# Kernel tuning notes

Hardware: AMD Instinct MI355X
Metric: run time of the kernel (lower is better)

## Reference

```python
import jax, jax.numpy as jnp
import numpy as np
from math import comb

# --- module hyperparameters (from init_kwargs / module-level constants) ---
F = 32          # features
NITER = 3       # num_iterations
NB = 16         # num_basis_functions
NDCM = 4        # n_dcm
CUTOFF = 4.0
MAXZ = 17       # max_atomic_number
NC = 9          # (max_degree+1)^2 spherical components, max_degree=2
DEG = np.array([0, 1, 1, 1, 2, 2, 2, 2, 2])  # degree l of each component
BINOM = jnp.asarray([comb(NB - 1, k) for k in range(NB)], dtype=jnp.float32)


def _np_sph9(x, y, z):
    # real spherical harmonics up to l=2 on the unit sphere (numpy, for Gaunt table)
    c0 = 0.28209479177387814; c1 = 0.4886025119029199
    c2a = 1.0925484305920792; c2b = 0.31539156525252005; c2c = 0.5462742152960396
    return np.stack([c0 * np.ones_like(x), c1 * y, c1 * z, c1 * x,
                     c2a * x * y, c2a * y * z, c2b * (3.0 * z * z - 1.0),
                     c2a * x * z, c2c * (x * x - y * y)], axis=0)


def _gaunt():
    # real Gaunt (Clebsch-Gordan-type) coefficients G[a,b,c] = int Y_a Y_b Y_c dOmega
    # via Gauss-Legendre (cos theta) x midpoint (phi) quadrature -- exact for l<=2 products
    ct, wt = np.polynomial.legendre.leggauss(64)
    nph = 256
    phi = (np.arange(nph) + 0.5) * (2.0 * np.pi / nph)
    st = np.sqrt(1.0 - ct ** 2)
    x = st[:, None] * np.cos(phi)[None, :]
    y = st[:, None] * np.sin(phi)[None, :]
    z = np.broadcast_to(ct[:, None], x.shape)
    w = (wt[:, None] * (2.0 * np.pi / nph)) * np.ones((1, nph))
    Y = _np_sph9(x, y, z)
    G = np.einsum('aij,bij,cij,ij->abc', Y, Y, Y, w)
    G[np.abs(G) < 1e-6] = 0.0
    return G

CG = jnp.asarray(_gaunt(), dtype=jnp.float32)  # (9, 9, 9), sparse


def _sph9(u):
    # u: (E, 3) unit vectors -> (E, 9)
    x, y, z = u[:, 0], u[:, 1], u[:, 2]
    c0 = 0.28209479177387814; c1 = 0.4886025119029199
    c2a = 1.0925484305920792; c2b = 0.31539156525252005; c2c = 0.5462742152960396
    return jnp.stack([jnp.full_like(x, c0), c1 * y, c1 * z, c1 * x,
                      c2a * x * y, c2a * y * z, c2b * (3.0 * z * z - 1.0),
                      c2a * x * z, c2c * (x * x - y * y)], axis=-1)


def _radial(r):
    # reciprocal Bernstein radial basis * smooth cutoff; r: (E,) -> (E, NB)
    u = 1.0 / (1.0 + r)
    k = jnp.arange(NB, dtype=jnp.float32)
    rb = BINOM * u[:, None] ** k * (1.0 - u[:, None]) ** (NB - 1 - k)
    t = r / CUTOFF
    den = jnp.where(t < 1.0, 1.0 - t * t, 1.0)
    fc = jnp.where(t < 1.0, jnp.exp(-t * t / den), 0.0)  # smooth_cutoff
    return rb * fc[:, None]


def _equiv_dense(x, W, b=None):
    # per-degree linear (equivariant Dense): x (N, 9, Fin), W (3, Fin, Fout); bias on l=0 only
    y = jnp.einsum('ncf,cfg->ncg', x, W[DEG])
    if b is not None:
        y = y.at[:, 0, :].add(b)
    return y


def _tp(xs, bf):
    # Gaunt tensor-product contraction: out[e,c,f] = sum_ab CG[a,b,c] xs[e,a,f] bf[e,b,f]
    # loop over the 9 fixed output components to avoid an (E,9,9,F) intermediate
    out = []
    for c in range(NC):
        t = jnp.einsum('eaf,ab->ebf', xs, CG[:, :, c])
        out.append(jnp.sum(t * bf, axis=1))
    return jnp.stack(out, axis=1)


def _forward(atomic_numbers, positions, dst_idx, src_idx, embed, Wb, W1, b1, W2, b2,
             Wt00, Wt11, Wmono, element_bias):
    n = atomic_numbers.shape[0]
    disp = positions[src_idx] - positions[dst_idx]                 # (E, 3) gather
    r = jnp.sqrt(jnp.sum(disp * disp, axis=-1) + 1e-12)            # safe norm
    u = disp / r[:, None]
    basis = _sph9(u)[:, :, None] * _radial(r)[:, None, :]          # (E, 9, NB)
    x = jnp.zeros((n, NC, F), dtype=positions.dtype).at[:, 0, :].set(embed[atomic_numbers])
    for i in range(NITER):  # message passing iterations
        bf = jnp.einsum('ebn,bng->ebg', basis, Wb[i][DEG])         # per-degree radial->feature mix (E,9,F)
        msg = _tp(x[src_idx], bf)                                  # gather src + tensor product
        y = x + jax.ops.segment_sum(msg, dst_idx, num_segments=n)  # scatter-aggregate + residual add
        y = _equiv_dense(y, W1[i], b1[i])
        y = jax.nn.silu(y)
        y = _equiv_dense(y, W2[i], b2[i])
        x = x + y                                                  # residual update
    # TensorDense to n_dcm channels, then readout heads
    mono = (x[:, 0, :] @ Wt00) @ Wmono + element_bias[atomic_numbers][:, None]  # (N, NDCM)
    dip = jnp.einsum('ncf,fg->ncg', x[:, 1:4, :], Wt11)            # (N, 3, NDCM) vector channel
    dip = jnp.clip(jax.nn.silu(dip), -0.3, 0.3) + positions[:, :, None]
    return mono, dip


def setup_inputs():
    key = jax.random.key(0)
    ks = jax.random.split(key, 12)
    N, E = 10000, 160000
    return {
        'atomic_numbers': jax.random.randint(ks[0], (N,), 0, MAXZ + 1),
        'positions': jax.random.normal(ks[1], (N, 3), jnp.float32) * 3.0,
        'dst_idx': jax.random.randint(ks[2], (E,), 0, N),
        'src_idx': jax.random.randint(ks[3], (E,), 0, N),
        'embed': jax.random.normal(ks[4], (MAXZ + 1, F), jnp.float32),
        'Wb': jax.random.normal(ks[5], (NITER, 3, NB, F), jnp.float32) / np.sqrt(NB).astype(np.float32),
        'W1': jax.random.normal(ks[6], (NITER, 3, F, F), jnp.float32) / np.sqrt(F).astype(np.float32),
        'b1': jnp.zeros((NITER, F), jnp.float32),
        'W2': jax.random.normal(ks[7], (NITER, 3, F, F), jnp.float32) / np.sqrt(F).astype(np.float32),
        'b2': jnp.zeros((NITER, F), jnp.float32),
        'Wt00': jax.random.normal(ks[8], (F, NDCM), jnp.float32) / np.sqrt(F).astype(np.float32),
        'Wt11': jax.random.normal(ks[9], (F, NDCM), jnp.float32) / np.sqrt(F).astype(np.float32),
        'Wmono': jax.random.normal(ks[10], (NDCM, NDCM), jnp.float32) / np.sqrt(NDCM).astype(np.float32),
        'element_bias': jnp.zeros((MAXZ + 1,), jnp.float32),
    }


def reference(atomic_numbers, positions, dst_idx, src_idx, embed, Wb, W1, b1, W2, b2,
              Wt00, Wt11, Wmono, element_bias):
    return _forward(atomic_numbers, positions, dst_idx, src_idx, embed, Wb, W1, b1, W2, b2,
                    Wt00, Wt11, Wmono, element_bias)
```

## Files before the change

kernel.cpp:

```cpp
#include <hip/hip_runtime.h>
#include <hip/hip_bf16.h>


#define NITER 3
#define BCAP  64

#define OFF_WB    0
#define OFF_W1    4608
#define OFF_B1    13824
#define OFF_W2    13920
#define OFF_B2    23136
#define OFF_WT00  23232
#define OFF_WT11  23360
#define OFF_WMONO 23488
#define OFF_EB    23504
#define OFF_EMB   23522
#define WC_TOTAL  24098

__device__ __forceinline__ float b2f(const __hip_bfloat16 v) { return __bfloat162float(v); }

#define KC0 0.28209479177387814f
#define KG1 0.21850968611841584f
#define KG2 0.12615662610100802f
#define KG3 0.18022375157287861f
#define KG4 0.09011187578643931f
#define KG5 0.15607834722743988f

__device__ __forceinline__ float ldany(const void* p, int i, bool f32) {
    return f32 ? ((const float*)p)[i] : b2f(((const __hip_bfloat16*)p)[i]);
}

__device__ __forceinline__ bool wave_sniff(const void* pos) {
    const __hip_bfloat16* p = (const __hip_bfloat16*)pos;
    int lane = threadIdx.x & 63;
    int bad = 0;
    #pragma unroll
    for (int k = 0; k < 4; k++) {
        float v = b2f(p[lane + k*64]);
        bad |= !(fabsf(v) < 1.0e6f);
    }
    return __ballot(bad) != 0ull;
}

__device__ __forceinline__ float xadd32(float v) {
    return v + __int_as_float(__shfl_xor(__float_as_int(v), 32, 64));
}

__device__ __forceinline__ bool edge_geom(float dx, float dy, float dz,
                                          float* sp, float* rad) {
    float r2 = dx*dx + dy*dy + dz*dz + 1e-12f;
    if (r2 >= 16.0f) return false;
    float r  = sqrtf(r2);
    float t2 = r2 * 0.0625f;
    float fc = __expf(-t2 / (1.0f - t2));
    float u = 1.0f / (1.0f + r);
    float v = 1.0f - u;
    const float BIN[16] = {1.f,15.f,105.f,455.f,1365.f,3003.f,5005.f,6435.f,
                           6435.f,5005.f,3003.f,1365.f,455.f,105.f,15.f,1.f};
    float vp[16];
    vp[0] = 1.0f;
    #pragma unroll
    for (int k = 1; k < 16; k++) vp[k] = vp[k-1] * v;
    float up = 1.0f;
    #pragma unroll
    for (int n = 0; n < 16; n++) { rad[n] = BIN[n] * up * vp[15-n] * fc; up *= u; }
    float ir = 1.0f / r;
    float ux = dx*ir, uy = dy*ir, uz = dz*ir;
    const float c0 = 0.28209479177387814f, c1 = 0.4886025119029199f;
    const float c2a = 1.0925484305920792f, c2b = 0.31539156525252005f, c2c = 0.5462742152960396f;
    sp[0] = c0;
    sp[1] = c1*uy; sp[2] = c1*uz; sp[3] = c1*ux;
    sp[4] = c2a*ux*uy; sp[5] = c2a*uy*uz; sp[6] = c2b*(3.0f*uz*uz - 1.0f);
    sp[7] = c2a*ux*uz; sp[8] = c2c*(ux*ux - uy*uy);
    return true;
}

__device__ __forceinline__ void write_geo_slot(float* gp, int s,
                                               const float* sp, const float* rad) {
    float4* g4 = (float4*)gp;
    g4[0] = make_float4(__int_as_float(s), 0.f, sp[0], sp[1]);
    g4[1] = make_float4(sp[2], sp[3], sp[4], sp[5]);
    g4[2] = make_float4(sp[6], sp[7], sp[8], 0.f);
    g4[4] = make_float4(rad[0],  rad[1],  rad[2],  rad[3]);
    g4[5] = make_float4(rad[4],  rad[5],  rad[6],  rad[7]);
    g4[6] = make_float4(rad[8],  rad[9],  rad[10], rad[11]);
    g4[7] = make_float4(rad[12], rad[13], rad[14], rad[15]);
}

template <bool FIRST, bool LAST>
__global__ __launch_bounds__(256) void iter_kernel(
        const float* __restrict__ xin, float* __restrict__ xout,
        const float* __restrict__ geo2, const int* __restrict__ cur,
        const float* __restrict__ Wbi,
        const float* __restrict__ W1i, const float* __restrict__ b1i,
        const float* __restrict__ W2i, const float* __restrict__ b2i,
        const int* __restrict__ an, const float* __restrict__ posf,
        const float* __restrict__ wc, const void* __restrict__ pos,
        void* __restrict__ out_, int N) {
    constexpr int NCH = LAST ? 4 : 9;
    constexpr int NR  = LAST ? 2 : 5;
    __shared__ float sm[4][9][33];
    bool f32o = false;
    if (LAST) f32o = wave_sniff(pos);
    int tid   = threadIdx.x;
    int wslot = tid >> 6;
    int lane  = tid & 63;
    int f     = lane & 31;
    int half  = lane >> 5;
    int n     = blockIdx.x * 4 + wslot;
    bool act  = (n < N);
    float (*tile)[33] = sm[wslot];

    float w0[16], w1[16], w2[16];
    #pragma unroll
    for (int k = 0; k < 16; k++) {
        w0[k] = Wbi[(0*16 + k)*32 + f];
        w1[k] = Wbi[(1*16 + k)*32 + f];
        w2[k] = Wbi[(2*16 + k)*32 + f];
    }
    float A0=0.f,A1=0.f,A2=0.f,A3=0.f,A4=0.f,A5=0.f,A6=0.f,A7=0.f,A8=0.f;
    if (act) {
        int beg = n * BCAP, end = beg + cur[n];
        for (int e = beg + half; e < end; e += 2) {
            const float4* gp = (const float4*)(geo2 + (size_t)e * 32);
            float4 h0 = gp[0], h1 = gp[1], h2 = gp[2];
            float4 r0 = gp[4], r1 = gp[5], r2 = gp[6], r3 = gp[7];
            int s = __float_as_int(h0.x);
            float rad[16] = {r0.x,r0.y,r0.z,r0.w, r1.x,r1.y,r1.z,r1.w,
                             r2.x,r2.y,r2.z,r2.w, r3.x,r3.y,r3.z,r3.w};
            float rw0 = 0.f, rw1 = 0.f, rw2 = 0.f;
            #pragma unroll
            for (int k = 0; k < 16; k++) {
                rw0 = fmaf(rad[k], w0[k], rw0);
                rw1 = fmaf(rad[k], w1[k], rw1);
                rw2 = fmaf(rad[k], w2[k], rw2);
            }
            float B0 = h0.z*rw0;
            float B1 = h0.w*rw1, B2 = h1.x*rw1, B3 = h1.y*rw1;
            float B4 = h1.z*rw2, B5 = h1.w*rw2, B6 = h2.x*rw2,
                  B7 = h2.y*rw2, B8 = h2.z*rw2;
            const float* xp = xin + (size_t)s*288 + f;
            if (FIRST) {
                float X0 = xp[0];
                float k0 = KC0 * X0;
                A0 += k0*B0; A1 += k0*B1; A2 += k0*B2; A3 += k0*B3; A4 += k0*B4;
                A5 += k0*B5; A6 += k0*B6; A7 += k0*B7; A8 += k0*B8;
            } else {
                float X0 = xp[0],   X1 = xp[32],  X2 = xp[64],  X3 = xp[96],  X4 = xp[128];
                float X5 = xp[160], X6 = xp[192], X7 = xp[224], X8 = xp[256];
                A0 += KC0*(X0*B0 + X1*B1 + X2*B2 + X3*B3 + X4*B4 + X5*B5 + X6*B6 + X7*B7 + X8*B8);
                A1 += KC0*(X0*B1 + X1*B0) + KG1*(X3*B4 + X4*B3 + X2*B5 + X5*B2)
                    - KG2*(X1*B6 + X6*B1) - KG1*(X1*B8 + X8*B1);
                A2 += KC0*(X0*B2 + X2*B0) + KG1*(X1*B5 + X5*B1 + X3*B7 + X7*B3)
                    + 2.0f*KG2*(X2*B6 + X6*B2);
                A3 += KC0*(X0*B3 + X3*B0) + KG1*(X1*B4 + X4*B1 + X2*B7 + X7*B2)
                    - KG2*(X3*B6 + X6*B3) + KG1*(X3*B8 + X8*B3);
                if (!LAST) {
                    A4 += KC0*(X0*B4 + X4*B0) + KG1*(X1*B3 + X3*B1) + KG5*(X5*B7 + X7*B5)
                        - KG3*(X4*B6 + X6*B4);
                    A5 += KC0*(X0*B5 + X5*B0) + KG1*(X1*B2 + X2*B1) + KG5*(X4*B7 + X7*B4)
                        + KG4*(X5*B6 + X6*B5) - KG5*(X5*B8 + X8*B5);
                    A6 += KC0*(X0*B6 + X6*B0) - KG2*X1*B1 + 2.0f*KG2*X2*B2 - KG2*X3*B3
                        - KG3*X4*B4 + KG4*X5*B5 + KG3*X6*B6 + KG4*X7*B7 - KG3*X8*B8;
                    A7 += KC0*(X0*B7 + X7*B0) + KG1*(X2*B3 + X3*B2) + KG5*(X4*B5 + X5*B4)
                        + KG4*(X6*B7 + X7*B6) + KG5*(X7*B8 + X8*B7);
                    A8 += KC0*(X0*B8 + X8*B0) - KG1*X1*B1 + KG1*X3*B3 - KG5*X5*B5 + KG5*X7*B7
                        - KG3*(X6*B8 + X8*B6);
                }
            }
        }
    }
    A0 = xadd32(A0); A1 = xadd32(A1); A2 = xadd32(A2); A3 = xadd32(A3);
    if (!LAST) {
        A4 = xadd32(A4); A5 = xadd32(A5); A6 = xadd32(A6);
        A7 = xadd32(A7); A8 = xadd32(A8);
    }

    float xr[9];
    #pragma unroll
    for (int c = 0; c < 9; c++) xr[c] = 0.f;
    if (act) {
        if (FIRST) {
            xr[0] = xin[(size_t)n*288 + f];
        } else {
            #pragma unroll
            for (int c = 0; c < NCH; c++) xr[c] = xin[(size_t)n*288 + c*32 + f];
        }
    }

    if (act && half == 0) {
        tile[0][f] = xr[0] + A0;
        tile[1][f] = xr[1] + A1;
        tile[2][f] = xr[2] + A2;
        tile[3][f] = xr[3] + A3;
        if (!LAST) {
            tile[4][f] = xr[4] + A4;
            tile[5][f] = xr[5] + A5;
            tile[6][f] = xr[6] + A6;
            tile[7][f] = xr[7] + A7;
            tile[8][f] = xr[8] + A8;
        }
    }
    __syncthreads();

    int g = f;
    float o1[NR];
    #pragma unroll
    for (int cc = 0; cc < NR; cc++) {
        int c  = cc*2 + half;
        int cs = (c < NCH) ? c : 0;
        int d  = (cs == 0) ? 0 : ((cs < 4) ? 1 : 2);
        const float* W1p = W1i + d * 1024;
        float acc = (c == 0) ? b1i[g] : 0.f;
        #pragma unroll
        for (int fi = 0; fi < 32; fi++)
            acc = fmaf(tile[cs][fi], W1p[fi*32 + g], acc);
        acc = acc * __builtin_amdgcn_rcpf(1.0f + __expf(-acc));
        o1[cc] = acc;
    }
    __syncthreads();
    #pragma unroll
    for (int cc = 0; cc < NR; cc++) {
        int c = cc*2 + half;
        if (c < NCH) tile[c][g] = o1[cc];
    }
    __syncthreads();

    #pragma unroll
    for (int cc = 0; cc < NR; cc++) {
        int c  = cc*2 + half;
        int cs = (c < NCH) ? c : 0;
        int d  = (cs == 0) ? 0 : ((cs < 4) ? 1 : 2);
        const float* W2p = W2i + d * 1024;
        float acc = (c == 0) ? b2i[g] : 0.f;
        #pragma unroll
        for (int fi = 0; fi < 32; fi++)
            acc = fmaf(tile[cs][fi], W2p[fi*32 + g], acc);
        float xf = xr[cs] + acc;
        if (!LAST) {
            if (act && c < NCH)
                xout[(size_t)n*288 + c*32 + g] = xf;
        } else if (act) {
            const float* WT = (c == 0) ? (wc + OFF_WT00) : (wc + OFF_WT11);
            float p0 = xf * WT[g*4 + 0];
            float p1 = xf * WT[g*4 + 1];
            float p2 = xf * WT[g*4 + 2];
            float p3 = xf * WT[g*4 + 3];
            #pragma unroll
            for (int m = 1; m <= 16; m <<= 1) {
                p0 += __shfl_xor(p0, m, 64);
                p1 += __shfl_xor(p1, m, 64);
                p2 += __shfl_xor(p2, m, 64);
                p3 += __shfl_xor(p3, m, 64);
            }
            if (g == 0) {
                if (c == 0) {
                    const float* Wmono = wc + OFF_WMONO;
                    float ebv = wc[OFF_EB + an[n]];
                    #pragma unroll
                    for (int m = 0; m < 4; m++) {
                        float a2 = ebv + p0*Wmono[0*4+m] + p1*Wmono[1*4+m]
                                       + p2*Wmono[2*4+m] + p3*Wmono[3*4+m];
                        if (f32o) ((float*)out_)[n*4 + m] = a2;
                        else ((__hip_bfloat16*)out_)[n*4 + m] = __float2bfloat16(a2);
                    }
                } else {
                    float pc = posf[n*3 + (c - 1)];
                    float pv[4] = {p0, p1, p2, p3};
                    #pragma unroll
                    for (int m = 0; m < 4; m++) {
                        float v = pv[m];
                        v = v * __builtin_amdgcn_rcpf(1.0f + __expf(-v));
                        v = fminf(fmaxf(v, -0.3f), 0.3f);
                        v += pc;
                        size_t o = (size_t)N*4 + (size_t)n*12 + (size_t)(c-1)*4 + m;
                        if (f32o) ((float*)out_)[o] = v;
                        else ((__hip_bfloat16*)out_)[o] = __float2bfloat16(v);
                    }
                }
            }
        }
    }
}

__global__ void setup_kernel(const void* pos, const void* Wb, const void* W1,
        const void* b1, const void* W2, const void* b2, const void* Wt00,
        const void* Wt11, const void* Wmono, const void* eb, const void* emb,
        const int* __restrict__ an,
        const int* __restrict__ srcI, const int* __restrict__ dstI,
        float* __restrict__ posf, float* __restrict__ wc,
        float* __restrict__ x, float* __restrict__ geo2, int* __restrict__ cur,
        int N, int E, int use_csr) {
    bool f32 = wave_sniff(pos);
    int i = blockIdx.x * blockDim.x + threadIdx.x;
    int np = N * 3;
    if (i < np) { posf[i] = ldany(pos, i, f32); return; }
    int j = i - np;
    if (j < WC_TOTAL) {
        const void* src; int rel;
        if      (j < OFF_W1)    { src = Wb;    rel = j; }
        else if (j < OFF_B1)    { src = W1;    rel = j - OFF_W1; }
        else if (j < OFF_W2)    { src = b1;    rel = j - OFF_B1; }
        else if (j < OFF_B2)    { src = W2;    rel = j - OFF_W2; }
        else if (j < OFF_WT00)  { src = b2;    rel = j - OFF_B2; }
        else if (j < OFF_WT11)  { src = Wt00;  rel = j - OFF_WT00; }
        else if (j < OFF_WMONO) { src = Wt11;  rel = j - OFF_WT11; }
        else if (j < OFF_EB)    { src = Wmono; rel = j - OFF_WMONO; }
        else if (j < OFF_EMB)   { src = eb;    rel = j - OFF_EB; }
        else                    { src = emb;   rel = j - OFF_EMB; }
        wc[j] = ldany(src, rel, f32);
        return;
    }
    j -= WC_TOTAL;
    if (j < N * 32) {
        int n = j >> 5, rem = j & 31;
        x[(size_t)n * 288 + rem] = ldany(emb, an[n] * 32 + rem, f32);
        return;
    }
    j -= N * 32;
    if (j < E && use_csr) {
        int s = srcI[j], d = dstI[j];
        float sp[9], rad[16];
        if (!edge_geom(ldany(pos, s*3+0, f32) - ldany(pos, d*3+0, f32),
                       ldany(pos, s*3+1, f32) - ldany(pos, d*3+1, f32),
                       ldany(pos, s*3+2, f32) - ldany(pos, d*3+2, f32),
                       sp, rad)) return;
        int slot = atomicAdd(&cur[d], 1);
        write_geo_slot(geo2 + ((size_t)d * BCAP + slot) * 32, s, sp, rad);
    }
}

template <bool FIRST>
__device__ __forceinline__ void atom_unit(
        const float* __restrict__ xin, float* __restrict__ xout,
        const float* __restrict__ y,
        const float* __restrict__ W1i, const float* __restrict__ b1i,
        const float* __restrict__ W2i, const float* __restrict__ b2i,
        int N, int t, int c, int lane, float* __restrict__ tile) {
    int d = (c == 0) ? 0 : ((c < 4) ? 1 : 2);
    const float* W1 = W1i + d * 1024;
    const float* W2 = W2i + d * 1024;
    bool usex = (!FIRST) || (c == 0);
    float4 xr4[8];
    #pragma unroll
    for (int k = 0; k < 8; k++) {
        int e  = lane * 4 + k * 256;
        int al = e >> 5, f = e & 31;
        int ag = t * 64 + al;
        float4 s = make_float4(0.f, 0.f, 0.f, 0.f);
        float4 xv = make_float4(0.f, 0.f, 0.f, 0.f);
        if (ag < N) {
            if (usex) xv = *(const float4*)(xin + (size_t)ag * 288 + c * 32 + f);
            float4 yv = *(const float4*)(y + (size_t)ag * 288 + c * 32 + f);
            s = make_float4(xv.x + yv.x, xv.y + yv.y, xv.z + yv.z, xv.w + yv.w);
        }
        xr4[k] = xv;
        *(float4*)(tile + al * 33 + f) = s;
    }
    __syncthreads();
    float yin[32];
    #pragma unroll
    for (int k = 0; k < 8; k++) {
        float4 v = *(const float4*)(tile + lane * 33 + 4 * k);
        yin[4*k+0] = v.x; yin[4*k+1] = v.y; yin[4*k+2] = v.z; yin[4*k+3] = v.w;
    }
    float acc[32];
    #pragma unroll
    for (int g = 0; g < 32; g++) acc[g] = (c == 0) ? b1i[g] : 0.0f;
    #pragma unroll 4
    for (int fi = 0; fi < 32; fi++) {
        float v = yin[fi];
        #pragma unroll
        for (int g = 0; g < 32; g++) acc[g] = fmaf(v, W1[fi*32 + g], acc[g]);
    }
    #pragma unroll
    for (int g = 0; g < 32; g++)
        acc[g] = acc[g] * __builtin_amdgcn_rcpf(1.0f + __expf(-acc[g]));
    float out[32];
    #pragma unroll
    for (int g = 0; g < 32; g++) out[g] = (c == 0) ? b2i[g] : 0.0f;
    #pragma unroll 4
    for (int fi = 0; fi < 32; fi++) {
        float v = acc[fi];
        #pragma unroll
        for (int g = 0; g < 32; g++) out[g] = fmaf(v, W2[fi*32 + g], out[g]);
    }
    __syncthreads();
    #pragma unroll
    for (int k = 0; k < 8; k++)
        *(float4*)(tile + lane * 33 + 4 * k) =
            make_float4(out[4*k+0], out[4*k+1], out[4*k+2], out[4*k+3]);
    __syncthreads();
    #pragma unroll
    for (int k = 0; k < 8; k++) {
        int e  = lane * 4 + k * 256;
        int al = e >> 5, f = e & 31;
        int ag = t * 64 + al;
        if (ag < N) {
            float4 dv = *(const float4*)(tile + al * 33 + f);
            float4 xv = xr4[k];
            *(float4*)(xout + (size_t)ag * 288 + c * 32 + f) =
                make_float4(xv.x + dv.x, xv.y + dv.y, xv.z + dv.z, xv.w + dv.w);
        }
    }
}

template <bool FIRST>
__global__ __launch_bounds__(256) void atom_kernel(
        float* __restrict__ x, const float* __restrict__ y,
        const float* __restrict__ W1i, const float* __restrict__ b1i,
        const float* __restrict__ W2i, const float* __restrict__ b2i,
        int N) {
    __shared__ float sm[4][64*33];
    int lane  = threadIdx.x & 63;
    int wslot = threadIdx.x >> 6;
    int u = __builtin_amdgcn_readfirstlane(blockIdx.x * 4 + wslot);
    int t = u / 9;
    int c = u - t * 9;
    atom_unit<FIRST>(x, x, y, W1i, b1i, W2i, b2i, N, t, c, lane, sm[wslot]);
}

__global__ void zero_kernel(float4* __restrict__ b, int n) {
    int i = blockIdx.x * blockDim.x + threadIdx.x;
    int stride = gridDim.x * blockDim.x;
    float4 z = make_float4(0.f, 0.f, 0.f, 0.f);
    for (; i < n; i += stride) b[i] = z;
}

__global__ __launch_bounds__(256) void edge_inline_kernel(
        const float* __restrict__ x, float* __restrict__ y,
        const float* __restrict__ posf,
        const int* __restrict__ srcI, const int* __restrict__ dstI,
        const float* __restrict__ Wbi, int E) {
    int f  = threadIdx.x & 31;
    int hw = (blockIdx.x * blockDim.x + threadIdx.x) >> 5;
    int nhw = gridDim.x * (blockDim.x >> 5);
    float w0[16], w1[16], w2[16];
    #pragma unroll
    for (int n = 0; n < 16; n++) {
        w0[n] = Wbi[(0*16 + n)*32 + f];
        w1[n] = Wbi[(1*16 + n)*32 + f];
        w2[n] = Wbi[(2*16 + n)*32 + f];
    }
    for (int e = hw; e < E; e += nhw) {
        int s = srcI[e], d = dstI[e];
        float sp[9], rad[16];
        if (!edge_geom(posf[s*3+0] - posf[d*3+0],
                       posf[s*3+1] - posf[d*3+1],
                       posf[s*3+2] - posf[d*3+2], sp, rad)) continue;
        float rw0 = 0.f, rw1 = 0.f, rw2 = 0.f;
        #pragma unroll
        for (int n = 0; n < 16; n++) {
            rw0 = fmaf(rad[n], w0[n], rw0);
            rw1 = fmaf(rad[n], w1[n], rw1);
            rw2 = fmaf(rad[n], w2[n], rw2);
        }
        float B0 = sp[0]*rw0;
        float B1 = sp[1]*rw1, B2 = sp[2]*rw1, B3 = sp[3]*rw1;
        float B4 = sp[4]*rw2, B5 = sp[5]*rw2, B6 = sp[6]*rw2,
              B7 = sp[7]*rw2, B8 = sp[8]*rw2;
        const float* xp = x + (size_t)s*288 + f;
        float X0 = xp[0],   X1 = xp[32],  X2 = xp[64],  X3 = xp[96],  X4 = xp[128];
        float X5 = xp[160], X6 = xp[192], X7 = xp[224], X8 = xp[256];
        float* yp = y + (size_t)d*288 + f;
        float m;
        m = KC0*(X0*B0 + X1*B1 + X2*B2 + X3*B3 + X4*B4 + X5*B5 + X6*B6 + X7*B7 + X8*B8);
        unsafeAtomicAdd(yp + 0, m);
        m = KC0*(X0*B1 + X1*B0) + KG1*(X3*B4 + X4*B3 + X2*B5 + X5*B2)
          - KG2*(X1*B6 + X6*B1) - KG1*(X1*B8 + X8*B1);
        unsafeAtomicAdd(yp + 32, m);
        m = KC0*(X0*B2 + X2*B0) + KG1*(X1*B5 + X5*B1 + X3*B7 + X7*B3)
          + 2.0f*KG2*(X2*B6 + X6*B2);
        unsafeAtomicAdd(yp + 64, m);
        m = KC0*(X0*B3 + X3*B0) + KG1*(X1*B4 + X4*B1 + X2*B7 + X7*B2)
          - KG2*(X3*B6 + X6*B3) + KG1*(X3*B8 + X8*B3);
        unsafeAtomicAdd(yp + 96, m);
        m = KC0*(X0*B4 + X4*B0) + KG1*(X1*B3 + X3*B1) + KG5*(X5*B7 + X7*B5)
          - KG3*(X4*B6 + X6*B4);
        unsafeAtomicAdd(yp + 128, m);
        m = KC0*(X0*B5 + X5*B0) + KG1*(X1*B2 + X2*B1) + KG5*(X4*B7 + X7*B4)
          + KG4*(X5*B6 + X6*B5) - KG5*(X5*B8 + X8*B5);
        unsafeAtomicAdd(yp + 160, m);
        m = KC0*(X0*B6 + X6*B0) - KG2*X1*B1 + 2.0f*KG2*X2*B2 - KG2*X3*B3
          - KG3*X4*B4 + KG4*X5*B5 + KG3*X6*B6 + KG4*X7*B7 - KG3*X8*B8;
        unsafeAtomicAdd(yp + 192, m);
        m = KC0*(X0*B7 + X7*B0) + KG1*(X2*B3 + X3*B2) + KG5*(X4*B5 + X5*B4)
          + KG4*(X6*B7 + X7*B6) + KG5*(X7*B8 + X8*B7);
        unsafeAtomicAdd(yp + 224, m);
        m = KC0*(X0*B8 + X8*B0) - KG1*X1*B1 + KG1*X3*B3 - KG5*X5*B5 + KG5*X7*B7
          - KG3*(X6*B8 + X8*B6);
        unsafeAtomicAdd(yp + 256, m);
    }
}

__global__ void readout_kernel(const float* __restrict__ x,
        const int* __restrict__ an, const float* __restrict__ posf,
        const float* __restrict__ wc, const void* __restrict__ pos,
        void* __restrict__ out, int N) {
    bool f32 = wave_sniff(pos);
    int n = blockIdx.x * blockDim.x + threadIdx.x;
    if (n >= N) return;
    const float* Wt00  = wc + OFF_WT00;
    const float* Wt11  = wc + OFF_WT11;
    const float* Wmono = wc + OFF_WMONO;
    const float* xb = x + (size_t)n * 288;
    float q[4] = {0.f, 0.f, 0.f, 0.f};
    for (int f = 0; f < 32; f++) {
        float xv = xb[f];
        #pragma unroll
        for (int j = 0; j < 4; j++) q[j] = fmaf(xv, Wt00[f*4 + j], q[j]);
    }
    float ebv = wc[OFF_EB + an[n]];
    #pragma unroll
    for (int m = 0; m < 4; m++) {
        float acc = ebv;
        #pragma unroll
        for (int j = 0; j < 4; j++) acc = fmaf(q[j], Wmono[j*4 + m], acc);
        if (f32) ((float*)out)[n*4 + m] = acc;
        else ((__hip_bfloat16*)out)[n*4 + m] = __float2bfloat16(acc);
    }
    #pragma unroll
    for (int c = 0; c < 3; c++) {
        float pc = posf[n*3 + c];
        const float* xc = xb + (1 + c)*32;
        float dq[4] = {0.f, 0.f, 0.f, 0.f};
        for (int f = 0; f < 32; f++) {
            float xv = xc[f];
            #pragma unroll
            for (int m = 0; m < 4; m++) dq[m] = fmaf(xv, Wt11[f*4 + m], dq[m]);
        }
        #pragma unroll
        for (int m = 0; m < 4; m++) {
            float v = dq[m];
            v = v * __builtin_amdgcn_rcpf(1.0f + __expf(-v));
            v = fminf(fmaxf(v, -0.3f), 0.3f);
            v += pc;
            if (f32) ((float*)out)[N*4 + n*12 + c*4 + m] = v;
            else ((__hip_bfloat16*)out)[N*4 + n*12 + c*4 + m] = __float2bfloat16(v);
        }
    }
}

extern "C" void kernel_launch(void* const* d_in, const int* in_sizes, int n_in,
                              void* d_out, int out_size, void* d_ws, size_t ws_size,
                              hipStream_t stream) {
    const int* an    = (const int*)d_in[0];
    const void* pos  = d_in[1];
    const int* dstI  = (const int*)d_in[2];
    const int* srcI  = (const int*)d_in[3];
    const void* embed= d_in[4];
    const void* Wb   = d_in[5];
    const void* W1   = d_in[6];
    const void* b1   = d_in[7];
    const void* W2   = d_in[8];
    const void* b2   = d_in[9];
    const void* Wt00 = d_in[10];
    const void* Wt11 = d_in[11];
    const void* Wmono= d_in[12];
    const void* eb   = d_in[13];
    int N = in_sizes[0];
    int E = in_sizes[2];

    {
        float* x0   = (float*)d_ws;
        float* x1   = x0 + (size_t)N * 288;
        float* posf = x1 + (size_t)N * 288;
        float* wc   = posf + (size_t)N * 3;
        int* cur    = (int*)(wc + WC_TOTAL);
        uintptr_t ga = ((uintptr_t)(cur + N) + 127) & ~(uintptr_t)127;
        float* geo2 = (float*)ga;
        size_t need = (uintptr_t)(geo2 + (size_t)N * BCAP * 32) - (uintptr_t)d_ws;
        if (ws_size >= need) {
            hipMemsetAsync(cur, 0, sizeof(int) * (size_t)N, stream);
            int tot = N * 3 + WC_TOTAL + N * 32 + E;
            setup_kernel<<<(tot + 255)/256, 256, 0, stream>>>(
                pos, Wb, W1, b1, W2, b2, Wt00, Wt11, Wmono, eb, embed,
                an, srcI, dstI, posf, wc, x0, geo2, cur, N, E, 1);
            int gblocks = (N + 3) / 4;
            iter_kernel<true,false><<<gblocks, 256, 0, stream>>>(
                x0, x1, geo2, cur,
                wc + OFF_WB, wc + OFF_W1, wc + OFF_B1, wc + OFF_W2, wc + OFF_B2,
                an, posf, wc, pos, d_out, N);
            iter_kernel<false,false><<<gblocks, 256, 0, stream>>>(
                x1, x0, geo2, cur,
                wc + OFF_WB + 1536, wc + OFF_W1 + 3072, wc + OFF_B1 + 32,
                wc + OFF_W2 + 3072, wc + OFF_B2 + 32,
                an, posf, wc, pos, d_out, N);
            iter_kernel<false,true><<<gblocks, 256, 0, stream>>>(
                x0, nullptr, geo2, cur,
                wc + OFF_WB + 3072, wc + OFF_W1 + 6144, wc + OFF_B1 + 64,
                wc + OFF_W2 + 6144, wc + OFF_B2 + 64,
                an, posf, wc, pos, d_out, N);
            return;
        }
    }

    float* x    = (float*)d_ws;
    float* y    = x + (size_t)N * 288;
    float* posf = y + (size_t)N * 288;
    float* wc   = posf + (size_t)N * 3;
    int* cur    = (int*)(wc + WC_TOTAL);
    int ntiles = (N + 63) / 64;

    hipMemsetAsync(cur, 0, sizeof(int) * (size_t)N, stream);
    zero_kernel<<<512, 256, 0, stream>>>((float4*)x, N * 72);
    {
        int tot = N * 3 + WC_TOTAL + N * 32;
        setup_kernel<<<(tot + 255)/256, 256, 0, stream>>>(
            pos, Wb, W1, b1, W2, b2, Wt00, Wt11, Wmono, eb, embed,
            an, srcI, dstI, posf, wc, x, nullptr, cur, N, E, 0);
    }
    int ablocks = (ntiles * 9 + 3) / 4;
    for (int i = 0; i < NITER; i++) {
        zero_kernel<<<512, 256, 0, stream>>>((float4*)y, N * 72);
        edge_inline_kernel<<<2048, 256, 0, stream>>>(x, y, posf, srcI, dstI,
            wc + OFF_WB + (size_t)i*1536, E);
        atom_kernel<false><<<ablocks, 256, 0, stream>>>(x, y,
            wc + OFF_W1 + (size_t)i*3072, wc + OFF_B1 + (size_t)i*32,
            wc + OFF_W2 + (size_t)i*3072, wc + OFF_B2 + (size_t)i*32, N);
    }
    readout_kernel<<<(N + 255)/256, 256, 0, stream>>>(x, an, posf, wc, pos,
                                                      d_out, N);
}
```

Baseline: 224.1 us.

## Interleave node feature layout, split neighbor ranges, prefetch source indices, stage Wb in LDS

Node features move to a feature-major interleaved layout (12 floats per feature, 384 per node). Each neighbor gather then becomes two float4 loads plus a scalar load instead of nine strided loads. The first iteration reads a compact 32-float embedding buffer, and source indices move to a separate sidx array so the next index can be prefetched. Each half-wave now walks a contiguous half of the neighbor list, the radial weights Wb are staged in shared memory instead of registers, and launch bounds request higher occupancy. The cost is an extra LDS transpose and sync on output writes, plus more workspace.

```diff
diff --git a/kernel.cpp b/kernel.cpp
--- a/kernel.cpp
+++ b/kernel.cpp
@@ -75,12 +75,12 @@
     return true;
 }
 
-__device__ __forceinline__ void write_geo_slot(float* gp, int s,
+__device__ __forceinline__ void write_geo_slot(float* gp,
                                                const float* sp, const float* rad) {
     float4* g4 = (float4*)gp;
-    g4[0] = make_float4(__int_as_float(s), 0.f, sp[0], sp[1]);
-    g4[1] = make_float4(sp[2], sp[3], sp[4], sp[5]);
-    g4[2] = make_float4(sp[6], sp[7], sp[8], 0.f);
+    g4[0] = make_float4(sp[0], sp[1], sp[2], sp[3]);
+    g4[1] = make_float4(sp[4], sp[5], sp[6], sp[7]);
+    g4[2] = make_float4(sp[8], 0.f, 0.f, 0.f);
     g4[4] = make_float4(rad[0],  rad[1],  rad[2],  rad[3]);
     g4[5] = make_float4(rad[4],  rad[5],  rad[6],  rad[7]);
     g4[6] = make_float4(rad[8],  rad[9],  rad[10], rad[11]);
@@ -88,9 +88,10 @@
 }
 
 template <bool FIRST, bool LAST>
-__global__ __launch_bounds__(256) void iter_kernel(
+__global__ __launch_bounds__(256, 8) void iter_kernel(
         const float* __restrict__ xin, float* __restrict__ xout,
         const float* __restrict__ geo2, const int* __restrict__ cur,
+        const int* __restrict__ sidx,
         const float* __restrict__ Wbi,
         const float* __restrict__ W1i, const float* __restrict__ b1i,
         const float* __restrict__ W2i, const float* __restrict__ b2i,
@@ -99,7 +100,8 @@
         void* __restrict__ out_, int N) {
     constexpr int NCH = LAST ? 4 : 9;
     constexpr int NR  = LAST ? 2 : 5;
-    __shared__ float sm[4][9][33];
+    __shared__ float sw[1536];
+    __shared__ float sm[4][12][33];
     bool f32o = false;
     if (LAST) f32o = wave_sniff(pos);
     int tid   = threadIdx.x;
@@ -111,43 +113,53 @@
     bool act  = (n < N);
     float (*tile)[33] = sm[wslot];
 
-    float w0[16], w1[16], w2[16];
-    #pragma unroll
-    for (int k = 0; k < 16; k++) {
-        w0[k] = Wbi[(0*16 + k)*32 + f];
-        w1[k] = Wbi[(1*16 + k)*32 + f];
-        w2[k] = Wbi[(2*16 + k)*32 + f];
-    }
+    for (int i = tid; i < 1536; i += 256) sw[i] = Wbi[i];
+    __syncthreads();
+
     float A0=0.f,A1=0.f,A2=0.f,A3=0.f,A4=0.f,A5=0.f,A6=0.f,A7=0.f,A8=0.f;
     if (act) {
-        int beg = n * BCAP, end = beg + cur[n];
-        for (int e = beg + half; e < end; e += 2) {
+        int cnt = __builtin_amdgcn_readfirstlane(cur[n]);
+        int h0c = (cnt + 1) >> 1;
+        int beg = n * BCAP;
+        int b0  = beg + (half ? h0c : 0);
+        int b1e = beg + (half ? cnt : h0c);
+        int e = b0;
+        int s_cur = (e < b1e) ? sidx[e] : 0;
+        while (e < b1e) {
+            int s_nxt = (e + 1 < b1e) ? sidx[e + 1] : 0;
+            float X0, X1, X2, X3, X4, X5, X6, X7, X8;
+            if (FIRST) {
+                X0 = xin[(size_t)s_cur * 32 + f];
+                X1=X2=X3=X4=X5=X6=X7=X8=0.f;
+            } else {
+                const float* xp = xin + (size_t)s_cur * 384 + f * 12;
+                float4 xa = *(const float4*)(xp);
+                float4 xb = *(const float4*)(xp + 4);
+                X8 = xp[8];
+                X0=xa.x; X1=xa.y; X2=xa.z; X3=xa.w;
+                X4=xb.x; X5=xb.y; X6=xb.z; X7=xb.w;
+            }
             const float4* gp = (const float4*)(geo2 + (size_t)e * 32);
             float4 h0 = gp[0], h1 = gp[1], h2 = gp[2];
             float4 r0 = gp[4], r1 = gp[5], r2 = gp[6], r3 = gp[7];
-            int s = __float_as_int(h0.x);
             float rad[16] = {r0.x,r0.y,r0.z,r0.w, r1.x,r1.y,r1.z,r1.w,
                              r2.x,r2.y,r2.z,r2.w, r3.x,r3.y,r3.z,r3.w};
             float rw0 = 0.f, rw1 = 0.f, rw2 = 0.f;
             #pragma unroll
             for (int k = 0; k < 16; k++) {
-                rw0 = fmaf(rad[k], w0[k], rw0);
-                rw1 = fmaf(rad[k], w1[k], rw1);
-                rw2 = fmaf(rad[k], w2[k], rw2);
+                rw0 = fmaf(rad[k], sw[       k*32 + f], rw0);
+                rw1 = fmaf(rad[k], sw[ 512 + k*32 + f], rw1);
+                rw2 = fmaf(rad[k], sw[1024 + k*32 + f], rw2);
             }
-            float B0 = h0.z*rw0;
-            float B1 = h0.w*rw1, B2 = h1.x*rw1, B3 = h1.y*rw1;
-            float B4 = h1.z*rw2, B5 = h1.w*rw2, B6 = h2.x*rw2,
-                  B7 = h2.y*rw2, B8 = h2.z*rw2;
-            const float* xp = xin + (size_t)s*288 + f;
+            float B0 = h0.x*rw0;
+            float B1 = h0.y*rw1, B2 = h0.z*rw1, B3 = h0.w*rw1;
+            float B4 = h1.x*rw2, B5 = h1.y*rw2, B6 = h1.z*rw2,
+                  B7 = h1.w*rw2, B8 = h2.x*rw2;
             if (FIRST) {
-                float X0 = xp[0];
                 float k0 = KC0 * X0;
                 A0 += k0*B0; A1 += k0*B1; A2 += k0*B2; A3 += k0*B3; A4 += k0*B4;
                 A5 += k0*B5; A6 += k0*B6; A7 += k0*B7; A8 += k0*B8;
             } else {
-                float X0 = xp[0],   X1 = xp[32],  X2 = xp[64],  X3 = xp[96],  X4 = xp[128];
-                float X5 = xp[160], X6 = xp[192], X7 = xp[224], X8 = xp[256];
                 A0 += KC0*(X0*B0 + X1*B1 + X2*B2 + X3*B3 + X4*B4 + X5*B5 + X6*B6 + X7*B7 + X8*B8);
                 A1 += KC0*(X0*B1 + X1*B0) + KG1*(X3*B4 + X4*B3 + X2*B5 + X5*B2)
                     - KG2*(X1*B6 + X6*B1) - KG1*(X1*B8 + X8*B1);
@@ -168,6 +180,7 @@
                         - KG3*(X6*B8 + X8*B6);
                 }
             }
+            s_cur = s_nxt; e++;
         }
     }
     A0 = xadd32(A0); A1 = xadd32(A1); A2 = xadd32(A2); A3 = xadd32(A3);
@@ -181,10 +194,14 @@
     for (int c = 0; c < 9; c++) xr[c] = 0.f;
     if (act) {
         if (FIRST) {
-            xr[0] = xin[(size_t)n*288 + f];
+            xr[0] = xin[(size_t)n * 32 + f];
         } else {
-            #pragma unroll
-            for (int c = 0; c < NCH; c++) xr[c] = xin[(size_t)n*288 + c*32 + f];
+            const float* xp = xin + (size_t)n * 384 + f * 12;
+            float4 xa = *(const float4*)(xp);
+            float4 xb = *(const float4*)(xp + 4);
+            xr[0]=xa.x; xr[1]=xa.y; xr[2]=xa.z; xr[3]=xa.w;
+            xr[4]=xb.x; xr[5]=xb.y; xr[6]=xb.z; xr[7]=xb.w;
+            xr[8]=xp[8];
         }
     }
 
@@ -226,6 +243,7 @@
     }
     __syncthreads();
 
+    float xf[NR];
     #pragma unroll
     for (int cc = 0; cc < NR; cc++) {
         int c  = cc*2 + half;
@@ -236,22 +254,19 @@
         #pragma unroll
         for (int fi = 0; fi < 32; fi++)
             acc = fmaf(tile[cs][fi], W2p[fi*32 + g], acc);
-        float xf = xr[cs] + acc;
-        if (!LAST) {
-            if (act && c < NCH)
-                xout[(size_t)n*288 + c*32 + g] = xf;
-        } else if (act) {
+        xf[cc] = xr[cs] + acc;
+        if (LAST && act) {
             const float* WT = (c == 0) ? (wc + OFF_WT00) : (wc + OFF_WT11);
-            float p0 = xf * WT[g*4 + 0];
-            float p1 = xf * WT[g*4 + 1];
-            float p2 = xf * WT[g*4 + 2];
-            float p3 = xf * WT[g*4 + 3];
+            float v0 = xf[cc] * WT[g*4 + 0];
+            float v1 = xf[cc] * WT[g*4 + 1];
+            float v2 = xf[cc] * WT[g*4 + 2];
+            float v3 = xf[cc] * WT[g*4 + 3];
             #pragma unroll
             for (int m = 1; m <= 16; m <<= 1) {
-                p0 += __shfl_xor(p0, m, 64);
-                p1 += __shfl_xor(p1, m, 64);
-                p2 += __shfl_xor(p2, m, 64);
-                p3 += __shfl_xor(p3, m, 64);
+                v0 += __shfl_xor(v0, m, 64);
+                v1 += __shfl_xor(v1, m, 64);
+                v2 += __shfl_xor(v2, m, 64);
+                v3 += __shfl_xor(v3, m, 64);
             }
             if (g == 0) {
                 if (c == 0) {
@@ -259,14 +274,14 @@
                     float ebv = wc[OFF_EB + an[n]];
                     #pragma unroll
                     for (int m = 0; m < 4; m++) {
-                        float a2 = ebv + p0*Wmono[0*4+m] + p1*Wmono[1*4+m]
-                                       + p2*Wmono[2*4+m] + p3*Wmono[3*4+m];
+                        float a2 = ebv + v0*Wmono[0*4+m] + v1*Wmono[1*4+m]
+                                       + v2*Wmono[2*4+m] + v3*Wmono[3*4+m];
                         if (f32o) ((float*)out_)[n*4 + m] = a2;
                         else ((__hip_bfloat16*)out_)[n*4 + m] = __float2bfloat16(a2);
                     }
                 } else {
                     float pc = posf[n*3 + (c - 1)];
-                    float pv[4] = {p0, p1, p2, p3};
+                    float pv[4] = {v0, v1, v2, v3};
                     #pragma unroll
                     for (int m = 0; m < 4; m++) {
                         float v = pv[m];
@@ -281,6 +296,25 @@
             }
         }
     }
+    if (!LAST) {
+        __syncthreads();
+        #pragma unroll
+        for (int cc = 0; cc < NR; cc++) {
+            int c = cc*2 + half;
+            if (c < 9) tile[c][g] = xf[cc];
+        }
+        if (half == 1) { tile[9][g] = 0.f; tile[10][g] = 0.f; tile[11][g] = 0.f; }
+        __syncthreads();
+        if (act) {
+            float* xo = xout + (size_t)n * 384;
+            *(float4*)(xo + f*12 + half*4) =
+                make_float4(tile[half*4+0][f], tile[half*4+1][f],
+                            tile[half*4+2][f], tile[half*4+3][f]);
+            if (half == 0)
+                *(float4*)(xo + f*12 + 8) =
+                    make_float4(tile[8][f], tile[9][f], tile[10][f], tile[11][f]);
+        }
+    }
 }
 
 __global__ void setup_kernel(const void* pos, const void* Wb, const void* W1,
@@ -290,7 +324,7 @@
         const int* __restrict__ srcI, const int* __restrict__ dstI,
         float* __restrict__ posf, float* __restrict__ wc,
         float* __restrict__ x, float* __restrict__ geo2, int* __restrict__ cur,
-        int N, int E, int use_csr) {
+        int* __restrict__ sidx, int N, int E, int use_csr) {
     bool f32 = wave_sniff(pos);
     int i = blockIdx.x * blockDim.x + threadIdx.x;
     int np = N * 3;
@@ -314,7 +348,9 @@
     j -= WC_TOTAL;
     if (j < N * 32) {
         int n = j >> 5, rem = j & 31;
-        x[(size_t)n * 288 + rem] = ldany(emb, an[n] * 32 + rem, f32);
+        size_t o = use_csr ? ((size_t)n * 32 + rem)
+                           : ((size_t)n * 288 + rem);
+        x[o] = ldany(emb, an[n] * 32 + rem, f32);
         return;
     }
     j -= N * 32;
@@ -326,98 +362,9 @@
                        ldany(pos, s*3+2, f32) - ldany(pos, d*3+2, f32),
                        sp, rad)) return;
         int slot = atomicAdd(&cur[d], 1);
-        write_geo_slot(geo2 + ((size_t)d * BCAP + slot) * 32, s, sp, rad);
-    }
-}
-
-template <bool FIRST>
-__device__ __forceinline__ void atom_unit(
-        const float* __restrict__ xin, float* __restrict__ xout,
-        const float* __restrict__ y,
-        const float* __restrict__ W1i, const float* __restrict__ b1i,
-        const float* __restrict__ W2i, const float* __restrict__ b2i,
-        int N, int t, int c, int lane, float* __restrict__ tile) {
-    int d = (c == 0) ? 0 : ((c < 4) ? 1 : 2);
-    const float* W1 = W1i + d * 1024;
-    const float* W2 = W2i + d * 1024;
-    bool usex = (!FIRST) || (c == 0);
-    float4 xr4[8];
-    #pragma unroll
-    for (int k = 0; k < 8; k++) {
-        int e  = lane * 4 + k * 256;
-        int al = e >> 5, f = e & 31;
-        int ag = t * 64 + al;
-        float4 s = make_float4(0.f, 0.f, 0.f, 0.f);
-        float4 xv = make_float4(0.f, 0.f, 0.f, 0.f);
-        if (ag < N) {
-            if (usex) xv = *(const float4*)(xin + (size_t)ag * 288 + c * 32 + f);
-            float4 yv = *(const float4*)(y + (size_t)ag * 288 + c * 32 + f);
-            s = make_float4(xv.x + yv.x, xv.y + yv.y, xv.z + yv.z, xv.w + yv.w);
-        }
-        xr4[k] = xv;
-        *(float4*)(tile + al * 33 + f) = s;
-    }
-    __syncthreads();
-    float yin[32];
-    #pragma unroll
-    for (int k = 0; k < 8; k++) {
-        float4 v = *(const float4*)(tile + lane * 33 + 4 * k);
-        yin[4*k+0] = v.x; yin[4*k+1] = v.y; yin[4*k+2] = v.z; yin[4*k+3] = v.w;
-    }
-    float acc[32];
-    #pragma unroll
-    for (int g = 0; g < 32; g++) acc[g] = (c == 0) ? b1i[g] : 0.0f;
-    #pragma unroll 4
-    for (int fi = 0; fi < 32; fi++) {
-        float v = yin[fi];
-        #pragma unroll
-        for (int g = 0; g < 32; g++) acc[g] = fmaf(v, W1[fi*32 + g], acc[g]);
-    }
-    #pragma unroll
-    for (int g = 0; g < 32; g++)
-        acc[g] = acc[g] * __builtin_amdgcn_rcpf(1.0f + __expf(-acc[g]));
-    float out[32];
-    #pragma unroll
-    for (int g = 0; g < 32; g++) out[g] = (c == 0) ? b2i[g] : 0.0f;
-    #pragma unroll 4
-    for (int fi = 0; fi < 32; fi++) {
-        float v = acc[fi];
-        #pragma unroll
-        for (int g = 0; g < 32; g++) out[g] = fmaf(v, W2[fi*32 + g], out[g]);
-    }
-    __syncthreads();
-    #pragma unroll
-    for (int k = 0; k < 8; k++)
-        *(float4*)(tile + lane * 33 + 4 * k) =
-            make_float4(out[4*k+0], out[4*k+1], out[4*k+2], out[4*k+3]);
-    __syncthreads();
-    #pragma unroll
-    for (int k = 0; k < 8; k++) {
-        int e  = lane * 4 + k * 256;
-        int al = e >> 5, f = e & 31;
-        int ag = t * 64 + al;
-        if (ag < N) {
-            float4 dv = *(const float4*)(tile + al * 33 + f);
-            float4 xv = xr4[k];
-            *(float4*)(xout + (size_t)ag * 288 + c * 32 + f) =
-                make_float4(xv.x + dv.x, xv.y + dv.y, xv.z + dv.z, xv.w + dv.w);
-        }
-    }
-}
-
-template <bool FIRST>
-__global__ __launch_bounds__(256) void atom_kernel(
-        float* __restrict__ x, const float* __restrict__ y,
-        const float* __restrict__ W1i, const float* __restrict__ b1i,
-        const float* __restrict__ W2i, const float* __restrict__ b2i,
-        int N) {
-    __shared__ float sm[4][64*33];
-    int lane  = threadIdx.x & 63;
-    int wslot = threadIdx.x >> 6;
-    int u = __builtin_amdgcn_readfirstlane(blockIdx.x * 4 + wslot);
-    int t = u / 9;
-    int c = u - t * 9;
-    atom_unit<FIRST>(x, x, y, W1i, b1i, W2i, b2i, N, t, c, lane, sm[wslot]);
+        sidx[d * BCAP + slot] = s;
+        write_geo_slot(geo2 + ((size_t)d * BCAP + slot) * 32, sp, rad);
+    }
 }
 
 __global__ void zero_kernel(float4* __restrict__ b, int n) {
@@ -493,6 +440,85 @@
     }
 }
 
+__global__ __launch_bounds__(256) void atom_kernel(
+        float* __restrict__ x, const float* __restrict__ y,
+        const float* __restrict__ W1i, const float* __restrict__ b1i,
+        const float* __restrict__ W2i, const float* __restrict__ b2i,
+        int N) {
+    __shared__ float sm[4][64*33];
+    int lane  = threadIdx.x & 63;
+    int wslot = threadIdx.x >> 6;
+    int u = __builtin_amdgcn_readfirstlane(blockIdx.x * 4 + wslot);
+    int t = u / 9;
+    int c = u - t * 9;
+    int d = (c == 0) ? 0 : ((c < 4) ? 1 : 2);
+    const float* W1 = W1i + d * 1024;
+    const float* W2 = W2i + d * 1024;
+    float* tile = sm[wslot];
+    float4 xr4[8];
+    #pragma unroll
+    for (int k = 0; k < 8; k++) {
+        int e  = lane * 4 + k * 256;
+        int al = e >> 5, f = e & 31;
+        int ag = t * 64 + al;
+        float4 s = make_float4(0.f, 0.f, 0.f, 0.f);
+        float4 xv = make_float4(0.f, 0.f, 0.f, 0.f);
+        if (ag < N) {
+            xv = *(const float4*)(x + (size_t)ag * 288 + c * 32 + f);
+            float4 yv = *(const float4*)(y + (size_t)ag * 288 + c * 32 + f);
+            s = make_float4(xv.x + yv.x, xv.y + yv.y, xv.z + yv.z, xv.w + yv.w);
+        }
+        xr4[k] = xv;
+        *(float4*)(tile + al * 33 + f) = s;
+    }
+    __syncthreads();
+    float yin[32];
+    #pragma unroll
+    for (int k = 0; k < 8; k++) {
+        float4 v = *(const float4*)(tile + lane * 33 + 4 * k);
+        yin[4*k+0] = v.x; yin[4*k+1] = v.y; yin[4*k+2] = v.z; yin[4*k+3] = v.w;
+    }
+    float acc[32];
+    #pragma unroll
+    for (int g = 0; g < 32; g++) acc[g] = (c == 0) ? b1i[g] : 0.0f;
+    #pragma unroll 4
+    for (int fi = 0; fi < 32; fi++) {
+        float v = yin[fi];
+        #pragma unroll
+        for (int g = 0; g < 32; g++) acc[g] = fmaf(v, W1[fi*32 + g], acc[g]);
+    }
+    #pragma unroll
+    for (int g = 0; g < 32; g++)
+        acc[g] = acc[g] * __builtin_amdgcn_rcpf(1.0f + __expf(-acc[g]));
+    float out[32];
+    #pragma unroll
+    for (int g = 0; g < 32; g++) out[g] = (c == 0) ? b2i[g] : 0.0f;
+    #pragma unroll 4
+    for (int fi = 0; fi < 32; fi++) {
+        float v = acc[fi];
+        #pragma unroll
+        for (int g = 0; g < 32; g++) out[g] = fmaf(v, W2[fi*32 + g], out[g]);
+    }
+    __syncthreads();
+    #pragma unroll
+    for (int k = 0; k < 8; k++)
+        *(float4*)(tile + lane * 33 + 4 * k) =
+            make_float4(out[4*k+0], out[4*k+1], out[4*k+2], out[4*k+3]);
+    __syncthreads();
+    #pragma unroll
+    for (int k = 0; k < 8; k++) {
+        int e  = lane * 4 + k * 256;
+        int al = e >> 5, f = e & 31;
+        int ag = t * 64 + al;
+        if (ag < N) {
+            float4 dv = *(const float4*)(tile + al * 33 + f);
+            float4 xv = xr4[k];
+            *(float4*)(x + (size_t)ag * 288 + c * 32 + f) =
+                make_float4(xv.x + dv.x, xv.y + dv.y, xv.z + dv.z, xv.w + dv.w);
+        }
+    }
+}
+
 __global__ void readout_kernel(const float* __restrict__ x,
         const int* __restrict__ an, const float* __restrict__ posf,
         const float* __restrict__ wc, const void* __restrict__ pos,
@@ -562,12 +588,14 @@
     int E = in_sizes[2];
 
     {
-        float* x0   = (float*)d_ws;
-        float* x1   = x0 + (size_t)N * 288;
-        float* posf = x1 + (size_t)N * 288;
+        float* x0c  = (float*)d_ws;
+        float* x1   = x0c + (size_t)N * 32;
+        float* x2   = x1 + (size_t)N * 384;
+        float* posf = x2 + (size_t)N * 384;
         float* wc   = posf + (size_t)N * 3;
         int* cur    = (int*)(wc + WC_TOTAL);
-        uintptr_t ga = ((uintptr_t)(cur + N) + 127) & ~(uintptr_t)127;
+        int* sidx   = cur + N;
+        uintptr_t ga = ((uintptr_t)(sidx + (size_t)N * BCAP) + 127) & ~(uintptr_t)127;
         float* geo2 = (float*)ga;
         size_t need = (uintptr_t)(geo2 + (size_t)N * BCAP * 32) - (uintptr_t)d_ws;
         if (ws_size >= need) {
@@ -575,19 +603,19 @@
             int tot = N * 3 + WC_TOTAL + N * 32 + E;
             setup_kernel<<<(tot + 255)/256, 256, 0, stream>>>(
                 pos, Wb, W1, b1, W2, b2, Wt00, Wt11, Wmono, eb, embed,
-                an, srcI, dstI, posf, wc, x0, geo2, cur, N, E, 1);
+                an, srcI, dstI, posf, wc, x0c, geo2, cur, sidx, N, E, 1);
             int gblocks = (N + 3) / 4;
             iter_kernel<true,false><<<gblocks, 256, 0, stream>>>(
-                x0, x1, geo2, cur,
+                x0c, x1, geo2, cur, sidx,
                 wc + OFF_WB, wc + OFF_W1, wc + OFF_B1, wc + OFF_W2, wc + OFF_B2,
                 an, posf, wc, pos, d_out, N);
             iter_kernel<false,false><<<gblocks, 256, 0, stream>>>(
-                x1, x0, geo2, cur,
+                x1, x2, geo2, cur, sidx,
                 wc + OFF_WB + 1536, wc + OFF_W1 + 3072, wc + OFF_B1 + 32,
                 wc + OFF_W2 + 3072, wc + OFF_B2 + 32,
                 an, posf, wc, pos, d_out, N);
             iter_kernel<false,true><<<gblocks, 256, 0, stream>>>(
-                x0, nullptr, geo2, cur,
+                x2, nullptr, geo2, cur, sidx,
                 wc + OFF_WB + 3072, wc + OFF_W1 + 6144, wc + OFF_B1 + 64,
                 wc + OFF_W2 + 6144, wc + OFF_B2 + 64,
                 an, posf, wc, pos, d_out, N);
@@ -608,14 +636,14 @@
         int tot = N * 3 + WC_TOTAL + N * 32;
         setup_kernel<<<(tot + 255)/256, 256, 0, stream>>>(
             pos, Wb, W1, b1, W2, b2, Wt00, Wt11, Wmono, eb, embed,
-            an, srcI, dstI, posf, wc, x, nullptr, cur, N, E, 0);
+            an, srcI, dstI, posf, wc, x, nullptr, cur, nullptr, N, E, 0);
     }
     int ablocks = (ntiles * 9 + 3) / 4;
     for (int i = 0; i < NITER; i++) {
         zero_kernel<<<512, 256, 0, stream>>>((float4*)y, N * 72);
         edge_inline_kernel<<<2048, 256, 0, stream>>>(x, y, posf, srcI, dstI,
             wc + OFF_WB + (size_t)i*1536, E);
-        atom_kernel<false><<<ablocks, 256, 0, stream>>>(x, y,
+        atom_kernel<<<ablocks, 256, 0, stream>>>(x, y,
             wc + OFF_W1 + (size_t)i*3072, wc + OFF_B1 + (size_t)i*32,
             wc + OFF_W2 + (size_t)i*3072, wc + OFF_B2 + (size_t)i*32, N);
     }
```

Result: slower. 470.2 us (+109.8%).
